# Optimization experiments

Measured on AMD Instinct MI355X. Metric: run time of the kernel, lower is better.

## Reference

```python
import jax, jax.numpy as jnp
import numpy as np

N_ENT, E, M, STEPS, B, H, C = 500000, 128, 8, 3, 4096, 256, 16

def setup_inputs() -> dict:
    key = jax.random.key(0)
    ks = jax.random.split(key, 13)
    s = 0.05
    return {
        "entity_ids": jax.random.randint(ks[0], (B, STEPS + 1), 0, N_ENT),
        "module_ids": jax.random.randint(ks[1], (B, STEPS), 0, M),
        "embedding": jax.random.normal(ks[2], (N_ENT, E), jnp.float32),
        "W_in": jax.random.normal(ks[3], (M, E, E), jnp.float32) * s,
        "b_in": jax.random.normal(ks[4], (M, E), jnp.float32) * s,
        "W_bias": jax.random.normal(ks[5], (M, E, E), jnp.float32) * s,
        "b_bias": jax.random.normal(ks[6], (M, E), jnp.float32) * s,
        "W_f": jax.random.normal(ks[7], (M, 2 * E, E), jnp.float32) * s,
        "b_f": jax.random.normal(ks[8], (M, E), jnp.float32) * s,
        "W1": jax.random.normal(ks[9], (E, H), jnp.float32) * s,
        "b1": jax.random.normal(ks[10], (H,), jnp.float32) * s,
        "W2": jax.random.normal(ks[11], (H, C), jnp.float32) * s,
        "b2": jax.random.normal(ks[12], (C,), jnp.float32) * s,
    }

def reference(entity_ids, module_ids, embedding, W_in, b_in, W_bias, b_bias,
              W_f, b_f, W1, b1, W2, b2):
    # x: [B, E] embedding of each path's start entity
    x = embedding[entity_ids[:, 0]]

    def step(x, inputs):
        mid, eid = inputs                      # [B], [B]
        bias = embedding[eid]                  # [B, E]
        h_in = jax.nn.relu(jnp.einsum('be,beo->bo', x, W_in[mid]) + b_in[mid])
        h_bi = jax.nn.relu(jnp.einsum('be,beo->bo', bias, W_bias[mid]) + b_bias[mid])
        h = jnp.concatenate([h_in, h_bi], axis=1)  # [B, 2E]
        x_new = jnp.tanh(jnp.einsum('bf,bfo->bo', h, W_f[mid]) + b_f[mid])
        return x_new, None

    xs = (module_ids.T, entity_ids[:, 1:].T)   # [STEPS, B] each
    x, _ = jax.lax.scan(step, x, xs)

    # classifier: Linear -> ReLU -> Linear
    h = jax.nn.relu(x @ W1 + b1)
    return h @ W2 + b2
```

## Files before the change

### kernel.cpp

```cpp
#include <hip/hip_runtime.h>

#define BB      4096
#define EE      128
#define MM      8
#define NSTEPS  3
#define HH      256
#define CC      16

#define TS      16
#define FB      1024

#define NFRAGBLK 1096

#define NBMAX   (BB/TS + MM)
#define PREP_G  512
#define PREP_S  24
#define PREP_GRID (NFRAGBLK + PREP_G + PREP_S)

typedef __attribute__((ext_vector_type(8))) short  bf16x8;
typedef __attribute__((ext_vector_type(4))) float  f32x4;

__device__ __forceinline__ unsigned short bf16_rn(float v) {
    unsigned u = __float_as_uint(v);
    return (unsigned short)((u + 0x7FFFu + ((u >> 16) & 1u)) >> 16);
}
__device__ __forceinline__ float bf16_f(unsigned short h) {
    return __uint_as_float(((unsigned)h) << 16);
}
__device__ __forceinline__ void split8(const float* v, bf16x8& hi, bf16x8& lo) {
    #pragma unroll
    for (int i = 0; i < 8; i++) {
        unsigned short h = bf16_rn(v[i]);
        hi[i] = (short)h;
        lo[i] = (short)bf16_rn(v[i] - bf16_f(h));
    }
}
__device__ __forceinline__ void split1(float v, unsigned short& h, unsigned short& l) {
    h = bf16_rn(v);
    l = bf16_rn(v - bf16_f(h));
}
#define MFMA(a,b,c) __builtin_amdgcn_mfma_f32_16x16x32_bf16((a),(b),(c),0,0,0)
__device__ __forceinline__ f32x4 mfma3(bf16x8 ah, bf16x8 al, bf16x8 bh, bf16x8 bl, f32x4 c) {
    c = MFMA(ah, bh, c);
    c = MFMA(ah, bl, c);
    c = MFMA(al, bh, c);
    return c;
}

__global__ __launch_bounds__(512) void prep_kernel(
    const int*   __restrict__ entity_ids, const int* __restrict__ module_ids,
    const float* __restrict__ embedding,
    const float* __restrict__ W_in, const float* __restrict__ W_bias,
    const float* __restrict__ W_f,  const float* __restrict__ W1,
    const float* __restrict__ W2,
    unsigned short* __restrict__ wf,
    unsigned short* __restrict__ x0h, unsigned short* __restrict__ x0l,
    unsigned short* __restrict__ ebh, unsigned short* __restrict__ ebl,
    int* __restrict__ cnt, int* __restrict__ perm)
{
    const int vb = blockIdx.x, tid = threadIdx.x;
    if (vb < NFRAGBLK) {
        unsigned short* dhi = wf + (size_t)vb * FB;
        unsigned short* dlo = dhi + 512;
        const int el = tid;
        const int ln = el >> 3, j = el & 7;
        const int krel = ((ln >> 4) << 3) + j;
        const int nrel = ln & 15;
        float v;
        if (vb < 512) {
            const int bb = vb & 255;
            const int kc = bb & 3, nt = (bb >> 2) & 7, m = bb >> 5;
            const float* src = (vb < 256 ? W_in : W_bias) + (size_t)m * EE * EE;
            v = src[(size_t)(kc*32 + krel) * EE + nt*16 + nrel];
        } else if (vb < 1024) {
            const int bb = vb - 512;
            const int kc = bb & 7, nt = (bb >> 3) & 7, m = bb >> 6;
            v = W_f[(size_t)m * 2*EE*EE + (size_t)(kc*32 + krel) * EE + nt*16 + nrel];
        } else if (vb < 1088) {
            const int bb = vb - 1024;
            const int kc = bb & 3, nt = bb >> 2;
            v = W1[(size_t)(kc*32 + krel) * HH + nt*16 + nrel];
        } else {
            const int kc = vb - 1088;
            v = W2[(size_t)(kc*32 + krel) * CC + nrel];
        }
        split1(v, dhi[el], dlo[el]);
    } else if (vb < NFRAGBLK + PREP_G) {
        const int u = vb - NFRAGBLK;
        const int rloc = tid >> 4, cpart = tid & 15;
        const int rglob = u*32 + rloc;
        const int g = rglob >> 12;
        const int s = rglob & (BB-1);
        const int eid = entity_ids[s*(NSTEPS+1) + g];
        const float* src = embedding + (size_t)eid*EE + cpart*8;
        float vv[8];
        *(float4*)(vv)     = *(const float4*)(src);
        *(float4*)(vv + 4) = *(const float4*)(src + 4);
        bf16x8 hi, lo;
        split8(vv, hi, lo);
        unsigned short* dh = (g == 0 ? x0h : ebh + (size_t)(g-1)*BB*EE) + (size_t)s*EE + cpart*8;
        unsigned short* dl = (g == 0 ? x0l : ebl + (size_t)(g-1)*BB*EE) + (size_t)s*EE + cpart*8;
        *(bf16x8*)dh = hi;
        *(bf16x8*)dl = lo;
    } else {
        const int u = vb - NFRAGBLK - PREP_G;
        const int gid = u*512 + tid;
        const int lane = tid & 63;
        const int t = gid >> 12, s = gid & (BB-1);
        const int m = module_ids[s*NSTEPS + t];
        unsigned long long mybal = 0ull, lanebal = 0ull;
        #pragma unroll
        for (int k = 0; k < MM; k++) {
            const unsigned long long bk = __ballot(m == k);
            if (m == k)    mybal   = bk;
            if (lane == k) lanebal = bk;
        }
        int base = 0;
        if (lane < MM) base = atomicAdd(&cnt[t*MM + lane], __popcll(lanebal));
        const int mybase = __shfl(base, m);
        const unsigned long long below = (1ull << lane) - 1ull;
        const int rank = __popcll(mybal & below);
        perm[((t*MM + m) << 12) + mybase + rank] = s;
    }
}

__global__ __launch_bounds__(512, 2) void step_kernel(
    const int t,
    const unsigned short* __restrict__ x0h, const unsigned short* __restrict__ x0l,
    const unsigned short* __restrict__ ebh, const unsigned short* __restrict__ ebl,
    const float* __restrict__ b_in, const float* __restrict__ b_bias,
    const float* __restrict__ b_f,
    const float* __restrict__ b1v, const float* __restrict__ b2,
    const unsigned short* __restrict__ wf,
    const int*   __restrict__ cnt, const int* __restrict__ perm,
    unsigned short* __restrict__ xsh, unsigned short* __restrict__ xsl,
    float* __restrict__ out)
{
    const int bx = blockIdx.x, tid = threadIdx.x;
    const int lane = tid & 63, wave = tid >> 6;
    const int row16 = lane & 15, quad = lane >> 4;

    int creg[MM];
    #pragma unroll
    for (int k = 0; k < MM; k++) creg[k] = cnt[t*MM + k];
    int m = -1, pref = 0, cm = 0, acc = 0;
    #pragma unroll
    for (int k = 0; k < MM; k++) {
        const int nbk = (creg[k] + TS - 1) >> 4;
        if (m < 0 && bx < acc + nbk) { m = k; pref = acc; cm = creg[k]; }
        acc += nbk;
    }
    if (m < 0) return;
    const int chunk = bx - pref;

    __shared__ __align__(16) unsigned short hfh[8][512];
    __shared__ __align__(16) unsigned short hfl[8][512];
    __shared__ int   sids[TS];
    __shared__ float red[8][TS][CC];

    if (tid < TS) {
        const int sl = chunk*TS + tid;
        sids[tid] = (sl < cm) ? perm[((t*MM + m) << 12) + sl] : -1;
    }
    __syncthreads();

    const int sA  = sids[row16];
    const int sAc = sA < 0 ? 0 : sA;

    const unsigned short* xh_p = (t == 0 ? x0h : xsh) + (size_t)sAc*EE;
    const unsigned short* xl_p = (t == 0 ? x0l : xsl) + (size_t)sAc*EE;
    const unsigned short* eh_p = ebh + (size_t)t*BB*EE + (size_t)sAc*EE;
    const unsigned short* el_p = ebl + (size_t)t*BB*EE + (size_t)sAc*EE;

    bf16x8 xh[4], xl[4], eh[4], el_[4];
    #pragma unroll
    for (int kc = 0; kc < 4; kc++) {
        const int off = kc*32 + quad*8;
        xh[kc]  = *(const bf16x8*)(xh_p + off);
        xl[kc]  = *(const bf16x8*)(xl_p + off);
        eh[kc]  = *(const bf16x8*)(eh_p + off);
        el_[kc] = *(const bf16x8*)(el_p + off);
    }

    f32x4 aci = {0.f,0.f,0.f,0.f}, acb = {0.f,0.f,0.f,0.f};
    #pragma unroll
    for (int kc = 0; kc < 4; kc++) {
        const unsigned short* bI = wf + (size_t)((m*8 + wave)*4 + kc)*FB;
        const unsigned short* bBp = wf + (size_t)(256 + (m*8 + wave)*4 + kc)*FB;
        const bf16x8 wih = *(const bf16x8*)(bI + lane*8);
        const bf16x8 wil = *(const bf16x8*)(bI + 512 + lane*8);
        const bf16x8 wbh = *(const bf16x8*)(bBp + lane*8);
        const bf16x8 wbl = *(const bf16x8*)(bBp + 512 + lane*8);
        aci = mfma3(xh[kc], xl[kc], wih, wil, aci);
        acb = mfma3(eh[kc], el_[kc], wbh, wbl, acb);
    }

    {
        const int col = wave*16 + row16;
        const float bin = b_in [m*EE + col];
        const float bbi = b_bias[m*EE + col];
        #pragma unroll
        for (int r = 0; r < 4; r++) {
            const int row = quad*4 + r;
            {
                const float v = fmaxf(aci[r] + bin, 0.f);
                const int k = col, kc = k >> 5;
                const int idx = (row + 16*((k >> 3) & 3))*8 + (k & 7);
                split1(v, hfh[kc][idx], hfl[kc][idx]);
            }
            {
                const float v = fmaxf(acb[r] + bbi, 0.f);
                const int k = EE + col, kc = k >> 5;
                const int idx = (row + 16*((k >> 3) & 3))*8 + (k & 7);
                split1(v, hfh[kc][idx], hfl[kc][idx]);
            }
        }
    }
    __syncthreads();

    f32x4 acf = {0.f,0.f,0.f,0.f};
    #pragma unroll
    for (int kc = 0; kc < 8; kc++) {
        const bf16x8 ah = *(const bf16x8*)(&hfh[kc][lane*8]);
        const bf16x8 al = *(const bf16x8*)(&hfl[kc][lane*8]);
        const unsigned short* bF = wf + (size_t)(512 + (m*8 + wave)*8 + kc)*FB;
        const bf16x8 wfh = *(const bf16x8*)(bF + lane*8);
        const bf16x8 wfl = *(const bf16x8*)(bF + 512 + lane*8);
        acf = mfma3(ah, al, wfh, wfl, acf);
    }

    const int col = wave*16 + row16;
    const float bfv = b_f[m*EE + col];
    float xv[4];
    #pragma unroll
    for (int r = 0; r < 4; r++) xv[r] = tanhf(acf[r] + bfv);

    if (t < NSTEPS-1) {
        #pragma unroll
        for (int r = 0; r < 4; r++) {
            const int s = sids[quad*4 + r];
            if (s >= 0) {
                unsigned short h, l;
                split1(xv[r], h, l);
                xsh[(size_t)s*EE + col] = h;
                xsl[(size_t)s*EE + col] = l;
            }
        }
    } else {
        __syncthreads();
        #pragma unroll
        for (int r = 0; r < 4; r++) {
            const int row = quad*4 + r;
            const int k = col, kc = k >> 5;
            const int idx = (row + 16*((k >> 3) & 3))*8 + (k & 7);
            split1(xv[r], hfh[kc][idx], hfl[kc][idx]);
        }
        __syncthreads();

        f32x4 a1[2] = {{0.f,0.f,0.f,0.f},{0.f,0.f,0.f,0.f}};
        #pragma unroll
        for (int i = 0; i < 2; i++) {
            const int nt = wave + 8*i;
            #pragma unroll
            for (int kc = 0; kc < 4; kc++) {
                const unsigned short* bW = wf + (size_t)(1024 + nt*4 + kc)*FB;
                const bf16x8 wh = *(const bf16x8*)(bW + lane*8);
                const bf16x8 wl = *(const bf16x8*)(bW + 512 + lane*8);
                const bf16x8 ah = *(const bf16x8*)(&hfh[kc][lane*8]);
                const bf16x8 al = *(const bf16x8*)(&hfl[kc][lane*8]);
                a1[i] = mfma3(ah, al, wh, wl, a1[i]);
            }
        }
        __syncthreads();
        #pragma unroll
        for (int i = 0; i < 2; i++) {
            const int c2 = (wave + 8*i)*16 + row16;
            const float b = b1v[c2];
            #pragma unroll
            for (int r = 0; r < 4; r++) {
                const int row = quad*4 + r;
                const float v = fmaxf(a1[i][r] + b, 0.f);
                const int kc = c2 >> 5;
                const int idx = (row + 16*((c2 >> 3) & 3))*8 + (c2 & 7);
                split1(v, hfh[kc][idx], hfl[kc][idx]);
            }
        }
        __syncthreads();

        f32x4 a2 = {0.f,0.f,0.f,0.f};
        {
            const int kc = wave;
            const bf16x8 ah = *(const bf16x8*)(&hfh[kc][lane*8]);
            const bf16x8 al = *(const bf16x8*)(&hfl[kc][lane*8]);
            const unsigned short* bW = wf + (size_t)(1088 + kc)*FB;
            const bf16x8 wh = *(const bf16x8*)(bW + lane*8);
            const bf16x8 wl = *(const bf16x8*)(bW + 512 + lane*8);
            a2 = mfma3(ah, al, wh, wl, a2);
        }
        #pragma unroll
        for (int r = 0; r < 4; r++) red[wave][quad*4 + r][row16] = a2[r];
        __syncthreads();

        if (tid < TS*CC) {
            const int sr = sids[tid >> 4];
            if (sr >= 0) {
                const int c = tid & 15;
                float v = b2[c];
                #pragma unroll
                for (int w = 0; w < 8; w++) v += red[w][tid >> 4][c];
                out[(size_t)sr*CC + c] = v;
            }
        }
    }
}

extern "C" void kernel_launch(void* const* d_in, const int* in_sizes, int n_in,
                              void* d_out, int out_size, void* d_ws, size_t ws_size,
                              hipStream_t stream) {
    const int*   entity_ids = (const int*)  d_in[0];
    const int*   module_ids = (const int*)  d_in[1];
    const float* embedding  = (const float*)d_in[2];
    const float* W_in   = (const float*)d_in[3];
    const float* b_in   = (const float*)d_in[4];
    const float* W_bias = (const float*)d_in[5];
    const float* b_bias = (const float*)d_in[6];
    const float* W_f    = (const float*)d_in[7];
    const float* b_f    = (const float*)d_in[8];
    const float* W1     = (const float*)d_in[9];
    const float* b1     = (const float*)d_in[10];
    const float* W2     = (const float*)d_in[11];
    const float* b2     = (const float*)d_in[12];
    float* out = (float*)d_out;

    char* ws = (char*)d_ws;
    int* cnt  = (int*)(ws + 0);
    int* perm = (int*)(ws + 4096);
    unsigned short* wfb = (unsigned short*)(ws + (1u<<20));
    unsigned short* x0h = (unsigned short*)(ws + (4u<<20));
    unsigned short* x0l = (unsigned short*)(ws + (5u<<20));
    unsigned short* xsh = (unsigned short*)(ws + (6u<<20));
    unsigned short* xsl = (unsigned short*)(ws + (7u<<20));
    unsigned short* ebh = (unsigned short*)(ws + (8u<<20));
    unsigned short* ebl = (unsigned short*)(ws + (11u<<20));

    hipMemsetAsync(cnt, 0, NSTEPS*MM*sizeof(int), stream);
    prep_kernel<<<PREP_GRID, 512, 0, stream>>>(entity_ids, module_ids, embedding,
                                               W_in, W_bias, W_f, W1, W2,
                                               wfb, x0h, x0l, ebh, ebl, cnt, perm);
    for (int t = 0; t < NSTEPS; t++) {
        step_kernel<<<NBMAX, 512, 0, stream>>>(t, x0h, x0l, ebh, ebl,
                                               b_in, b_bias, b_f, b1, b2,
                                               wfb, cnt, perm, xsh, xsl, out);
    }
}
```

Measured before the change: 355.2 us.

## Fuse step kernels into one persistent kernel with per-row flag sync

Replaces the three per-step launches with a single cooperative persistent kernel of 256 blocks that loops over the steps. Ordering between steps is kept by per-sample flags with release/acquire atomics instead of kernel boundaries. The embedding gather and bf16 hi/lo split are moved from the prep kernel into the step kernel, removing the staged ebh/ebl buffers and their extra memory round trip. Module bucketing now uses per-segment counts without global atomics, so the memset is dropped. The cost is spin-waiting and a two-pass grid that assumes at most 512 tiles per step. Forward progress also depends on all blocks being co-resident.

```diff
diff --git a/kernel.cpp b/kernel.cpp
--- a/kernel.cpp
+++ b/kernel.cpp
@@ -12,10 +12,9 @@
 
 #define NFRAGBLK 1096
 
-#define NBMAX   (BB/TS + MM)
-#define PREP_G  512
-#define PREP_S  24
-#define PREP_GRID (NFRAGBLK + PREP_G + PREP_S)
+#define NSEG    8
+#define GRIDN   256
+#define PREP_GRID (NFRAGBLK + NSTEPS*NSEG + 8)
 
 typedef __attribute__((ext_vector_type(8))) short  bf16x8;
 typedef __attribute__((ext_vector_type(4))) float  f32x4;
@@ -48,17 +47,16 @@
 }
 
 __global__ __launch_bounds__(512) void prep_kernel(
-    const int*   __restrict__ entity_ids, const int* __restrict__ module_ids,
-    const float* __restrict__ embedding,
+    const int*   __restrict__ module_ids,
     const float* __restrict__ W_in, const float* __restrict__ W_bias,
     const float* __restrict__ W_f,  const float* __restrict__ W1,
     const float* __restrict__ W2,
     unsigned short* __restrict__ wf,
-    unsigned short* __restrict__ x0h, unsigned short* __restrict__ x0l,
-    unsigned short* __restrict__ ebh, unsigned short* __restrict__ ebl,
-    int* __restrict__ cnt, int* __restrict__ perm)
+    int* __restrict__ wcnt, int* __restrict__ perm, int* __restrict__ fl)
 {
     const int vb = blockIdx.x, tid = threadIdx.x;
+    __shared__ int wc8[8][MM];
+
     if (vb < NFRAGBLK) {
         unsigned short* dhi = wf + (size_t)vb * FB;
         unsigned short* dlo = dhi + 512;
@@ -85,28 +83,11 @@
             v = W2[(size_t)(kc*32 + krel) * CC + nrel];
         }
         split1(v, dhi[el], dlo[el]);
-    } else if (vb < NFRAGBLK + PREP_G) {
+    } else if (vb < NFRAGBLK + NSTEPS*NSEG) {
         const int u = vb - NFRAGBLK;
-        const int rloc = tid >> 4, cpart = tid & 15;
-        const int rglob = u*32 + rloc;
-        const int g = rglob >> 12;
-        const int s = rglob & (BB-1);
-        const int eid = entity_ids[s*(NSTEPS+1) + g];
-        const float* src = embedding + (size_t)eid*EE + cpart*8;
-        float vv[8];
-        *(float4*)(vv)     = *(const float4*)(src);
-        *(float4*)(vv + 4) = *(const float4*)(src + 4);
-        bf16x8 hi, lo;
-        split8(vv, hi, lo);
-        unsigned short* dh = (g == 0 ? x0h : ebh + (size_t)(g-1)*BB*EE) + (size_t)s*EE + cpart*8;
-        unsigned short* dl = (g == 0 ? x0l : ebl + (size_t)(g-1)*BB*EE) + (size_t)s*EE + cpart*8;
-        *(bf16x8*)dh = hi;
-        *(bf16x8*)dl = lo;
-    } else {
-        const int u = vb - NFRAGBLK - PREP_G;
-        const int gid = u*512 + tid;
-        const int lane = tid & 63;
-        const int t = gid >> 12, s = gid & (BB-1);
+        const int t = u >> 3, seg = u & 7;
+        const int lane = tid & 63, wave = tid >> 6;
+        const int s = seg*512 + tid;
         const int m = module_ids[s*NSTEPS + t];
         unsigned long long mybal = 0ull, lanebal = 0ull;
         #pragma unroll
@@ -115,200 +96,270 @@
             if (m == k)    mybal   = bk;
             if (lane == k) lanebal = bk;
         }
+        if (lane < MM) wc8[wave][lane] = __popcll(lanebal);
+        __syncthreads();
         int base = 0;
-        if (lane < MM) base = atomicAdd(&cnt[t*MM + lane], __popcll(lanebal));
-        const int mybase = __shfl(base, m);
+        #pragma unroll
+        for (int w = 0; w < 8; w++) if (w < wave) base += wc8[w][m];
         const unsigned long long below = (1ull << lane) - 1ull;
         const int rank = __popcll(mybal & below);
-        perm[((t*MM + m) << 12) + mybase + rank] = s;
+        perm[(((t*MM + m)*NSEG) + seg)*512 + base + rank] = s;
+        if (tid < MM) {
+            int sum = 0;
+            #pragma unroll
+            for (int w = 0; w < 8; w++) sum += wc8[w][tid];
+            wcnt[((t*MM + tid)*NSEG) + seg] = sum;
+        }
+    } else {
+        const int u = vb - NFRAGBLK - NSTEPS*NSEG;
+        fl[u*512 + tid] = 0;
     }
 }
 
-__global__ __launch_bounds__(512, 2) void step_kernel(
-    const int t,
-    const unsigned short* __restrict__ x0h, const unsigned short* __restrict__ x0l,
-    const unsigned short* __restrict__ ebh, const unsigned short* __restrict__ ebl,
+__global__ __launch_bounds__(512, 2) void steps_kernel(
+    const int*   __restrict__ entity_ids,
+    const float* __restrict__ embedding,
     const float* __restrict__ b_in, const float* __restrict__ b_bias,
     const float* __restrict__ b_f,
     const float* __restrict__ b1v, const float* __restrict__ b2,
     const unsigned short* __restrict__ wf,
-    const int*   __restrict__ cnt, const int* __restrict__ perm,
+    const int* __restrict__ wcnt, const int* __restrict__ perm,
     unsigned short* __restrict__ xsh, unsigned short* __restrict__ xsl,
-    float* __restrict__ out)
+    int* __restrict__ fl, float* __restrict__ out)
 {
     const int bx = blockIdx.x, tid = threadIdx.x;
     const int lane = tid & 63, wave = tid >> 6;
     const int row16 = lane & 15, quad = lane >> 4;
 
-    int creg[MM];
-    #pragma unroll
-    for (int k = 0; k < MM; k++) creg[k] = cnt[t*MM + k];
-    int m = -1, pref = 0, cm = 0, acc = 0;
-    #pragma unroll
-    for (int k = 0; k < MM; k++) {
-        const int nbk = (creg[k] + TS - 1) >> 4;
-        if (m < 0 && bx < acc + nbk) { m = k; pref = acc; cm = creg[k]; }
-        acc += nbk;
-    }
-    if (m < 0) return;
-    const int chunk = bx - pref;
-
     __shared__ __align__(16) unsigned short hfh[8][512];
     __shared__ __align__(16) unsigned short hfl[8][512];
     __shared__ int   sids[TS];
     __shared__ float red[8][TS][CC];
 
-    if (tid < TS) {
-        const int sl = chunk*TS + tid;
-        sids[tid] = (sl < cm) ? perm[((t*MM + m) << 12) + sl] : -1;
-    }
-    __syncthreads();
-
-    const int sA  = sids[row16];
-    const int sAc = sA < 0 ? 0 : sA;
-
-    const unsigned short* xh_p = (t == 0 ? x0h : xsh) + (size_t)sAc*EE;
-    const unsigned short* xl_p = (t == 0 ? x0l : xsl) + (size_t)sAc*EE;
-    const unsigned short* eh_p = ebh + (size_t)t*BB*EE + (size_t)sAc*EE;
-    const unsigned short* el_p = ebl + (size_t)t*BB*EE + (size_t)sAc*EE;
-
-    bf16x8 xh[4], xl[4], eh[4], el_[4];
-    #pragma unroll
-    for (int kc = 0; kc < 4; kc++) {
-        const int off = kc*32 + quad*8;
-        xh[kc]  = *(const bf16x8*)(xh_p + off);
-        xl[kc]  = *(const bf16x8*)(xl_p + off);
-        eh[kc]  = *(const bf16x8*)(eh_p + off);
-        el_[kc] = *(const bf16x8*)(el_p + off);
-    }
-
-    f32x4 aci = {0.f,0.f,0.f,0.f}, acb = {0.f,0.f,0.f,0.f};
-    #pragma unroll
-    for (int kc = 0; kc < 4; kc++) {
-        const unsigned short* bI = wf + (size_t)((m*8 + wave)*4 + kc)*FB;
-        const unsigned short* bBp = wf + (size_t)(256 + (m*8 + wave)*4 + kc)*FB;
-        const bf16x8 wih = *(const bf16x8*)(bI + lane*8);
-        const bf16x8 wil = *(const bf16x8*)(bI + 512 + lane*8);
-        const bf16x8 wbh = *(const bf16x8*)(bBp + lane*8);
-        const bf16x8 wbl = *(const bf16x8*)(bBp + 512 + lane*8);
-        aci = mfma3(xh[kc], xl[kc], wih, wil, aci);
-        acb = mfma3(eh[kc], el_[kc], wbh, wbl, acb);
-    }
-
-    {
-        const int col = wave*16 + row16;
-        const float bin = b_in [m*EE + col];
-        const float bbi = b_bias[m*EE + col];
+    for (int t = 0; t < NSTEPS; t++) {
+        int tot[MM];
         #pragma unroll
-        for (int r = 0; r < 4; r++) {
-            const int row = quad*4 + r;
+        for (int k = 0; k < MM; k++) {
+            int s = 0;
+            #pragma unroll
+            for (int j = 0; j < NSEG; j++) s += wcnt[(t*MM + k)*NSEG + j];
+            tot[k] = s;
+        }
+        int NB = 0;
+        #pragma unroll
+        for (int k = 0; k < MM; k++) NB += (tot[k] + TS - 1) >> 4;
+
+        for (int pass = 0; pass < 2; pass++) {
+            const int vb = bx + pass*GRIDN;
+            if (vb >= NB) break;
+
+            int m = -1, pref = 0, cm = 0, acc = 0;
+            #pragma unroll
+            for (int k = 0; k < MM; k++) {
+                const int nbk = (tot[k] + TS - 1) >> 4;
+                if (m < 0 && vb < acc + nbk) { m = k; pref = acc; cm = tot[k]; }
+                acc += nbk;
+            }
+            const int chunk = vb - pref;
+
+            __syncthreads();
+            if (tid < TS) {
+                const int sl = chunk*TS + tid;
+                int sv = -1;
+                if (sl < cm) {
+                    int j = 0, r = sl;
+                    while (true) {
+                        const int c = wcnt[(t*MM + m)*NSEG + j];
+                        if (r < c) break;
+                        r -= c; j++;
+                    }
+                    sv = perm[((t*MM + m)*NSEG + j)*512 + r];
+                }
+                sids[tid] = sv;
+            }
+            __syncthreads();
+
+            const int sA  = sids[row16];
+            const int sAc = sA < 0 ? 0 : sA;
+
+            bf16x8 xh[4], xl[4], eh[4], el_[4];
+            const int eidb = entity_ids[sAc*(NSTEPS+1) + t + 1];
+            const float* srcb = embedding + (size_t)eidb*EE;
+
+            if (t == 0) {
+                const int eid0 = entity_ids[sAc*(NSTEPS+1)];
+                const float* src0 = embedding + (size_t)eid0*EE;
+                #pragma unroll
+                for (int kc = 0; kc < 4; kc++) {
+                    const int off = kc*32 + quad*8;
+                    float vv[8], bb[8];
+                    *(float4*)(vv)     = *(const float4*)(src0 + off);
+                    *(float4*)(vv + 4) = *(const float4*)(src0 + off + 4);
+                    *(float4*)(bb)     = *(const float4*)(srcb + off);
+                    *(float4*)(bb + 4) = *(const float4*)(srcb + off + 4);
+                    split8(vv, xh[kc], xl[kc]);
+                    split8(bb, eh[kc], el_[kc]);
+                }
+            } else {
+                float bb[4][8];
+                #pragma unroll
+                for (int kc = 0; kc < 4; kc++) {
+                    const int off = kc*32 + quad*8;
+                    *(float4*)(bb[kc])     = *(const float4*)(srcb + off);
+                    *(float4*)(bb[kc] + 4) = *(const float4*)(srcb + off + 4);
+                }
+                if (tid < TS && sids[tid] >= 0) {
+                    int* f = &fl[sids[tid]];
+                    while (__hip_atomic_load(f, __ATOMIC_RELAXED, __HIP_MEMORY_SCOPE_AGENT) < t)
+                        __builtin_amdgcn_s_sleep(2);
+                    (void)__hip_atomic_load(f, __ATOMIC_ACQUIRE, __HIP_MEMORY_SCOPE_AGENT);
+                }
+                __syncthreads();
+
+                const unsigned short* xhp = xsh + (size_t)sAc*EE;
+                const unsigned short* xlp = xsl + (size_t)sAc*EE;
+                #pragma unroll
+                for (int kc = 0; kc < 4; kc++) {
+                    const int off = kc*32 + quad*8;
+                    xh[kc] = *(const bf16x8*)(xhp + off);
+                    xl[kc] = *(const bf16x8*)(xlp + off);
+                    split8(bb[kc], eh[kc], el_[kc]);
+                }
+            }
+
+            f32x4 aci = {0.f,0.f,0.f,0.f}, acb = {0.f,0.f,0.f,0.f};
+            #pragma unroll
+            for (int kc = 0; kc < 4; kc++) {
+                const unsigned short* bI  = wf + (size_t)((m*8 + wave)*4 + kc)*FB;
+                const unsigned short* bBp = wf + (size_t)(256 + (m*8 + wave)*4 + kc)*FB;
+                const bf16x8 wih = *(const bf16x8*)(bI + lane*8);
+                const bf16x8 wil = *(const bf16x8*)(bI + 512 + lane*8);
+                const bf16x8 wbh = *(const bf16x8*)(bBp + lane*8);
+                const bf16x8 wbl = *(const bf16x8*)(bBp + 512 + lane*8);
+                aci = mfma3(xh[kc], xl[kc], wih, wil, aci);
+                acb = mfma3(eh[kc], el_[kc], wbh, wbl, acb);
+            }
+
             {
-                const float v = fmaxf(aci[r] + bin, 0.f);
-                const int k = col, kc = k >> 5;
-                const int idx = (row + 16*((k >> 3) & 3))*8 + (k & 7);
-                split1(v, hfh[kc][idx], hfl[kc][idx]);
-            }
-            {
-                const float v = fmaxf(acb[r] + bbi, 0.f);
-                const int k = EE + col, kc = k >> 5;
-                const int idx = (row + 16*((k >> 3) & 3))*8 + (k & 7);
-                split1(v, hfh[kc][idx], hfl[kc][idx]);
-            }
-        }
-    }
-    __syncthreads();
-
-    f32x4 acf = {0.f,0.f,0.f,0.f};
-    #pragma unroll
-    for (int kc = 0; kc < 8; kc++) {
-        const bf16x8 ah = *(const bf16x8*)(&hfh[kc][lane*8]);
-        const bf16x8 al = *(const bf16x8*)(&hfl[kc][lane*8]);
-        const unsigned short* bF = wf + (size_t)(512 + (m*8 + wave)*8 + kc)*FB;
-        const bf16x8 wfh = *(const bf16x8*)(bF + lane*8);
-        const bf16x8 wfl = *(const bf16x8*)(bF + 512 + lane*8);
-        acf = mfma3(ah, al, wfh, wfl, acf);
-    }
-
-    const int col = wave*16 + row16;
-    const float bfv = b_f[m*EE + col];
-    float xv[4];
-    #pragma unroll
-    for (int r = 0; r < 4; r++) xv[r] = tanhf(acf[r] + bfv);
-
-    if (t < NSTEPS-1) {
-        #pragma unroll
-        for (int r = 0; r < 4; r++) {
-            const int s = sids[quad*4 + r];
-            if (s >= 0) {
-                unsigned short h, l;
-                split1(xv[r], h, l);
-                xsh[(size_t)s*EE + col] = h;
-                xsl[(size_t)s*EE + col] = l;
-            }
-        }
-    } else {
-        __syncthreads();
-        #pragma unroll
-        for (int r = 0; r < 4; r++) {
-            const int row = quad*4 + r;
-            const int k = col, kc = k >> 5;
-            const int idx = (row + 16*((k >> 3) & 3))*8 + (k & 7);
-            split1(xv[r], hfh[kc][idx], hfl[kc][idx]);
-        }
-        __syncthreads();
-
-        f32x4 a1[2] = {{0.f,0.f,0.f,0.f},{0.f,0.f,0.f,0.f}};
-        #pragma unroll
-        for (int i = 0; i < 2; i++) {
-            const int nt = wave + 8*i;
-            #pragma unroll
-            for (int kc = 0; kc < 4; kc++) {
-                const unsigned short* bW = wf + (size_t)(1024 + nt*4 + kc)*FB;
-                const bf16x8 wh = *(const bf16x8*)(bW + lane*8);
-                const bf16x8 wl = *(const bf16x8*)(bW + 512 + lane*8);
+                const int col = wave*16 + row16;
+                const float bin = b_in [m*EE + col];
+                const float bbi = b_bias[m*EE + col];
+                #pragma unroll
+                for (int r = 0; r < 4; r++) {
+                    const int row = quad*4 + r;
+                    {
+                        const float v = fmaxf(aci[r] + bin, 0.f);
+                        const int k = col, kc = k >> 5;
+                        const int idx = (row + 16*((k >> 3) & 3))*8 + (k & 7);
+                        split1(v, hfh[kc][idx], hfl[kc][idx]);
+                    }
+                    {
+                        const float v = fmaxf(acb[r] + bbi, 0.f);
+                        const int k = EE + col, kc = k >> 5;
+                        const int idx = (row + 16*((k >> 3) & 3))*8 + (k & 7);
+                        split1(v, hfh[kc][idx], hfl[kc][idx]);
+                    }
+                }
+            }
+            __syncthreads();
+
+            f32x4 acf = {0.f,0.f,0.f,0.f};
+            #pragma unroll
+            for (int kc = 0; kc < 8; kc++) {
                 const bf16x8 ah = *(const bf16x8*)(&hfh[kc][lane*8]);
                 const bf16x8 al = *(const bf16x8*)(&hfl[kc][lane*8]);
-                a1[i] = mfma3(ah, al, wh, wl, a1[i]);
-            }
-        }
-        __syncthreads();
-        #pragma unroll
-        for (int i = 0; i < 2; i++) {
-            const int c2 = (wave + 8*i)*16 + row16;
-            const float b = b1v[c2];
-            #pragma unroll
-            for (int r = 0; r < 4; r++) {
-                const int row = quad*4 + r;
-                const float v = fmaxf(a1[i][r] + b, 0.f);
-                const int kc = c2 >> 5;
-                const int idx = (row + 16*((c2 >> 3) & 3))*8 + (c2 & 7);
-                split1(v, hfh[kc][idx], hfl[kc][idx]);
-            }
-        }
-        __syncthreads();
-
-        f32x4 a2 = {0.f,0.f,0.f,0.f};
-        {
-            const int kc = wave;
-            const bf16x8 ah = *(const bf16x8*)(&hfh[kc][lane*8]);
-            const bf16x8 al = *(const bf16x8*)(&hfl[kc][lane*8]);
-            const unsigned short* bW = wf + (size_t)(1088 + kc)*FB;
-            const bf16x8 wh = *(const bf16x8*)(bW + lane*8);
-            const bf16x8 wl = *(const bf16x8*)(bW + 512 + lane*8);
-            a2 = mfma3(ah, al, wh, wl, a2);
-        }
-        #pragma unroll
-        for (int r = 0; r < 4; r++) red[wave][quad*4 + r][row16] = a2[r];
-        __syncthreads();
-
-        if (tid < TS*CC) {
-            const int sr = sids[tid >> 4];
-            if (sr >= 0) {
-                const int c = tid & 15;
-                float v = b2[c];
-                #pragma unroll
-                for (int w = 0; w < 8; w++) v += red[w][tid >> 4][c];
-                out[(size_t)sr*CC + c] = v;
+                const unsigned short* bF = wf + (size_t)(512 + (m*8 + wave)*8 + kc)*FB;
+                const bf16x8 wfh = *(const bf16x8*)(bF + lane*8);
+                const bf16x8 wfl = *(const bf16x8*)(bF + 512 + lane*8);
+                acf = mfma3(ah, al, wfh, wfl, acf);
+            }
+
+            const int col = wave*16 + row16;
+            const float bfv = b_f[m*EE + col];
+            float xv[4];
+            #pragma unroll
+            for (int r = 0; r < 4; r++) xv[r] = tanhf(acf[r] + bfv);
+
+            if (t < NSTEPS-1) {
+                #pragma unroll
+                for (int r = 0; r < 4; r++) {
+                    const int s = sids[quad*4 + r];
+                    if (s >= 0) {
+                        unsigned short h, l;
+                        split1(xv[r], h, l);
+                        xsh[(size_t)s*EE + col] = h;
+                        xsl[(size_t)s*EE + col] = l;
+                    }
+                }
+                __syncthreads();
+                if (tid < TS && sids[tid] >= 0)
+                    __hip_atomic_store(&fl[sids[tid]], t+1,
+                                       __ATOMIC_RELEASE, __HIP_MEMORY_SCOPE_AGENT);
+            } else {
+                __syncthreads();
+                #pragma unroll
+                for (int r = 0; r < 4; r++) {
+                    const int row = quad*4 + r;
+                    const int k = col, kc = k >> 5;
+                    const int idx = (row + 16*((k >> 3) & 3))*8 + (k & 7);
+                    split1(xv[r], hfh[kc][idx], hfl[kc][idx]);
+                }
+                __syncthreads();
+
+                f32x4 a1[2] = {{0.f,0.f,0.f,0.f},{0.f,0.f,0.f,0.f}};
+                #pragma unroll
+                for (int i = 0; i < 2; i++) {
+                    const int nt = wave + 8*i;
+                    #pragma unroll
+                    for (int kc = 0; kc < 4; kc++) {
+                        const unsigned short* bW = wf + (size_t)(1024 + nt*4 + kc)*FB;
+                        const bf16x8 wh = *(const bf16x8*)(bW + lane*8);
+                        const bf16x8 wl = *(const bf16x8*)(bW + 512 + lane*8);
+                        const bf16x8 ah = *(const bf16x8*)(&hfh[kc][lane*8]);
+                        const bf16x8 al = *(const bf16x8*)(&hfl[kc][lane*8]);
+                        a1[i] = mfma3(ah, al, wh, wl, a1[i]);
+                    }
+                }
+                __syncthreads();
+                #pragma unroll
+                for (int i = 0; i < 2; i++) {
+                    const int c2 = (wave + 8*i)*16 + row16;
+                    const float b = b1v[c2];
+                    #pragma unroll
+                    for (int r = 0; r < 4; r++) {
+                        const int row = quad*4 + r;
+                        const float v = fmaxf(a1[i][r] + b, 0.f);
+                        const int kc = c2 >> 5;
+                        const int idx = (row + 16*((c2 >> 3) & 3))*8 + (c2 & 7);
+                        split1(v, hfh[kc][idx], hfl[kc][idx]);
+                    }
+                }
+                __syncthreads();
+
+                f32x4 a2 = {0.f,0.f,0.f,0.f};
+                {
+                    const int kc = wave;
+                    const bf16x8 ah = *(const bf16x8*)(&hfh[kc][lane*8]);
+                    const bf16x8 al = *(const bf16x8*)(&hfl[kc][lane*8]);
+                    const unsigned short* bW = wf + (size_t)(1088 + kc)*FB;
+                    const bf16x8 wh = *(const bf16x8*)(bW + lane*8);
+                    const bf16x8 wl = *(const bf16x8*)(bW + 512 + lane*8);
+                    a2 = mfma3(ah, al, wh, wl, a2);
+                }
+                #pragma unroll
+                for (int r = 0; r < 4; r++) red[wave][quad*4 + r][row16] = a2[r];
+                __syncthreads();
+
+                if (tid < TS*CC) {
+                    const int sr = sids[tid >> 4];
+                    if (sr >= 0) {
+                        const int c = tid & 15;
+                        float v = b2[c];
+                        #pragma unroll
+                        for (int w = 0; w < 8; w++) v += red[w][tid >> 4][c];
+                        out[(size_t)sr*CC + c] = v;
+                    }
+                }
             }
         }
     }
@@ -333,23 +384,26 @@
     float* out = (float*)d_out;
 
     char* ws = (char*)d_ws;
-    int* cnt  = (int*)(ws + 0);
+    int* wcnt = (int*)(ws + 0);
     int* perm = (int*)(ws + 4096);
+    int* fl   = (int*)(ws + (512u<<10));
     unsigned short* wfb = (unsigned short*)(ws + (1u<<20));
-    unsigned short* x0h = (unsigned short*)(ws + (4u<<20));
-    unsigned short* x0l = (unsigned short*)(ws + (5u<<20));
-    unsigned short* xsh = (unsigned short*)(ws + (6u<<20));
-    unsigned short* xsl = (unsigned short*)(ws + (7u<<20));
-    unsigned short* ebh = (unsigned short*)(ws + (8u<<20));
-    unsigned short* ebl = (unsigned short*)(ws + (11u<<20));
-
-    hipMemsetAsync(cnt, 0, NSTEPS*MM*sizeof(int), stream);
-    prep_kernel<<<PREP_GRID, 512, 0, stream>>>(entity_ids, module_ids, embedding,
+    unsigned short* xsh = (unsigned short*)(ws + (4u<<20));
+    unsigned short* xsl = (unsigned short*)(ws + (5u<<20));
+
+    prep_kernel<<<PREP_GRID, 512, 0, stream>>>(module_ids,
                                                W_in, W_bias, W_f, W1, W2,
-                                               wfb, x0h, x0l, ebh, ebl, cnt, perm);
-    for (int t = 0; t < NSTEPS; t++) {
-        step_kernel<<<NBMAX, 512, 0, stream>>>(t, x0h, x0l, ebh, ebl,
-                                               b_in, b_bias, b_f, b1, b2,
-                                               wfb, cnt, perm, xsh, xsl, out);
+                                               wfb, wcnt, perm, fl);
+
+    void* sargs[] = { &entity_ids, &embedding, &b_in, &b_bias, &b_f,
+                      &b1, &b2, &wfb, &wcnt, &perm, &xsh, &xsl, &fl, &out };
+    hipError_t e = hipLaunchCooperativeKernel(
+        reinterpret_cast<const void*>(steps_kernel),
+        dim3(GRIDN), dim3(512), sargs, 0u, stream);
+    if (e != hipSuccess) {
+        (void)hipGetLastError();
+        steps_kernel<<<GRIDN, 512, 0, stream>>>(entity_ids, embedding,
+                                                b_in, b_bias, b_f, b1, b2,
+                                                wfb, wcnt, perm, xsh, xsl, fl, out);
     }
 }
```

New measurement: 406.4 us. +14.4%, slower.
